# Kernel optimization log

Measured on AMD Instinct MI355X. Metric: run time of the kernel, lower is better.

The kernel has to match this reference:

```python
import jax, jax.numpy as jnp
import numpy as np

DIM = 1024
STATE = 256
B, S = 4, 4096

def setup_inputs() -> dict:
    key = jax.random.key(0)
    ks = jax.random.split(key, 8)
    sc_b = 1.0 / np.sqrt(DIM)
    sc_c = 1.0 / np.sqrt(STATE)
    return {
        "x": jax.random.normal(ks[0], (B, S, DIM), dtype=jnp.float32),
        "A": jax.random.normal(ks[1], (STATE,), dtype=jnp.float32) * 0.02,
        "B_w": jax.random.uniform(ks[2], (STATE, DIM), minval=-sc_b, maxval=sc_b),
        "B_b": jax.random.uniform(ks[3], (STATE,), minval=-sc_b, maxval=sc_b),
        "C_w": jax.random.uniform(ks[4], (DIM, STATE), minval=-sc_c, maxval=sc_c),
        "C_b": jax.random.uniform(ks[5], (DIM,), minval=-sc_c, maxval=sc_c),
        "D_w": jax.random.uniform(ks[6], (DIM, DIM), minval=-sc_b, maxval=sc_b),
        "D_b": jax.random.uniform(ks[7], (DIM,), minval=-sc_b, maxval=sc_b),
    }

def reference(x, A, B_w, B_b, C_w, C_b, D_w, D_b):
    # Precompute input projections in batch (the per-step loop only needs state*A + Bu)
    Bu = jnp.einsum('bsd,nd->bsn', x, B_w) + B_b          # [B,S,STATE]
    Du = jnp.einsum('bsd,ed->bse', x, D_w) + D_b          # [B,S,DIM]
    Aexp = jnp.exp(A)[None, :]                             # [1,STATE]
    state0 = jnp.zeros((x.shape[0], A.shape[0]), dtype=x.dtype)

    def step(state, bu_t):
        state = jnp.tanh(state * Aexp + bu_t)
        return state, state

    _, states = jax.lax.scan(step, state0, jnp.swapaxes(Bu, 0, 1))  # [S,B,STATE]
    states = jnp.swapaxes(states, 0, 1)                              # [B,S,STATE]
    y = jnp.einsum('bsn,en->bse', states, C_w) + C_b + Du
    return y
```

## Files before the change

### kernel.cpp

```cpp
#include <hip/hip_runtime.h>
#include <hip/hip_bf16.h>

#define DIM 1024
#define STATE 256
#define BATCH 4
#define SEQ 4096
#define M_TOT (BATCH * SEQ)

typedef short short8 __attribute__((ext_vector_type(8)));
typedef float f32x4 __attribute__((ext_vector_type(4)));

__device__ __forceinline__ unsigned short f2bf(float f) {
  unsigned int u = __float_as_uint(f);
  u += 0x7fff + ((u >> 16) & 1);
  return (unsigned short)(u >> 16);
}

__device__ __forceinline__ float bf2f(unsigned short u) {
  return __uint_as_float((unsigned int)u << 16);
}

__device__ __forceinline__ void gl_lds16(const void* g, void* l) {
  __builtin_amdgcn_global_load_lds(
      (const __attribute__((address_space(1))) void*)g,
      (__attribute__((address_space(3))) void*)l, 16, 0, 0);
}

#define C2F 2.8853900817779268f
#define LOG2EF 1.4426950408889634f
#define VMC(N) asm volatile("s_waitcnt vmcnt(" #N ")" ::: "memory")

__global__ __launch_bounds__(256) void convert_bw(
    const float* __restrict__ Bw, unsigned short* __restrict__ bwb) {
  const int r = blockIdx.x;
  const int c = threadIdx.x * 4;
  const float4 v = *(const float4*)(Bw + (size_t)r * DIM + c);
  *(ushort4*)(bwb + (size_t)r * DIM + c) =
      make_ushort4(f2bf(v.x), f2bf(v.y), f2bf(v.z), f2bf(v.w));
}

__global__ __launch_bounds__(256, 2) void gemm_GX(
    const float* __restrict__ x,
    const unsigned short* __restrict__ bwb,
    const float* __restrict__ Bb,
    const float* __restrict__ A,
    unsigned short* __restrict__ G,
    unsigned short* __restrict__ xb)
{
  __shared__ char lds[81920];

  const int tid = threadIdx.x;
  const int wave = tid >> 6;
  const int lane = tid & 63;
  const int lr = lane & 15;
  const int lk = lane >> 4;
  const int m0 = blockIdx.x * 32;

  f32x4 acc[2][4];
#pragma unroll
  for (int i = 0; i < 2; ++i)
#pragma unroll
    for (int j = 0; j < 4; ++j) acc[i][j] = (f32x4){0.f, 0.f, 0.f, 0.f};

  const char* xB  = (const char*)x;
  const char* bwB = (const char*)bwb;
  char* xbB = (char*)xb;

  auto stage = [&](int kt) {
    if (kt >= 16) return;
    char* slot = lds + (kt & 1) * 40960;
#pragma unroll
    for (int i = 0; i < 2; ++i) {
      const int s = i * 256 + tid;
      const int r = s >> 4;
      const int c = (s & 15) ^ (r & 7);
      gl_lds16(xB + (size_t)(m0 + r) * 4096 + (size_t)kt * 256 + c * 16,
               slot + i * 4096 + wave * 1024);
    }
#pragma unroll
    for (int i = 0; i < 8; ++i) {
      const int s = i * 256 + tid;
      const int r = s >> 3;
      const int c = (s & 7) ^ (r & 7);
      gl_lds16(bwB + (size_t)r * 2048 + (size_t)kt * 128 + c * 16,
               slot + 8192 + i * 4096 + wave * 1024);
    }
  };

  stage(0);
  VMC(0);
  __builtin_amdgcn_s_barrier();
  stage(1);

  for (int t = 0; t < 16; ++t) {
    const char* As = lds + (t & 1) * 40960;
    const char* Bs = As + 8192;

    short8 af[2][2];
#pragma unroll
    for (int kk = 0; kk < 2; ++kk)
#pragma unroll
      for (int f = 0; f < 2; ++f) {
        const int row = f * 16 + lr;
        const int sw = row & 7;
        const f32x4 a0 = *(const f32x4*)(As + row * 256 + (((kk * 8 + 2 * lk)     ^ sw) << 4));
        const f32x4 a1 = *(const f32x4*)(As + row * 256 + (((kk * 8 + 2 * lk + 1) ^ sw) << 4));
        short8 v;
#pragma unroll
        for (int j = 0; j < 4; ++j) {
          v[j]     = (short)f2bf(a0[j]);
          v[4 + j] = (short)f2bf(a1[j]);
        }
        af[kk][f] = v;
      }

    if ((t & 3) == wave) {
#pragma unroll
      for (int kk = 0; kk < 2; ++kk)
#pragma unroll
        for (int f = 0; f < 2; ++f) {
          const int row = f * 16 + lr;
          *(short8*)(xbB + (size_t)(m0 + row) * 2048 +
                     (size_t)t * 128 + kk * 64 + lk * 16) = af[kk][f];
        }
    }

    short8 bfr[2][4];
#pragma unroll
    for (int kk = 0; kk < 2; ++kk)
#pragma unroll
      for (int fj = 0; fj < 4; ++fj) {
        const int n = wave * 64 + fj * 16 + lr;
        bfr[kk][fj] = *(const short8*)(Bs + n * 128 + (((kk * 4 + lk) ^ (n & 7)) << 4));
      }
#pragma unroll
    for (int kk = 0; kk < 2; ++kk)
#pragma unroll
      for (int f = 0; f < 2; ++f)
#pragma unroll
        for (int fj = 0; fj < 4; ++fj)
          acc[f][fj] = __builtin_amdgcn_mfma_f32_16x16x32_bf16(
              af[kk][f], bfr[kk][fj], acc[f][fj], 0, 0, 0);

    if (t < 15) {
      VMC(0);
      __builtin_amdgcn_s_barrier();
      stage(t + 2);
    }
  }

#pragma unroll
  for (int fj = 0; fj < 4; ++fj) {
    const int cg = wave * 64 + fj * 16 + lr;
    const float bbv = fmaf(Bb[cg], C2F,
                           C2F * __builtin_amdgcn_exp2f(A[cg] * LOG2EF));
#pragma unroll
    for (int f = 0; f < 2; ++f)
#pragma unroll
      for (int j = 0; j < 4; ++j) {
        const int rg = m0 + f * 16 + lk * 4 + j;
        G[(size_t)rg * STATE + cg] = f2bf(fmaf(acc[f][fj][j], C2F, bbv));
      }
  }
}

__global__ __launch_bounds__(256) void scan_kernel(
    const unsigned short* __restrict__ G,
    const float* __restrict__ A,
    const float* __restrict__ Cw,
    const float* __restrict__ Dw,
    unsigned short* __restrict__ wob,
    unsigned short* __restrict__ states)
{
  const int tid = threadIdx.x;
  const int e0 = blockIdx.x * 4;
#pragma unroll
  for (int rr = 0; rr < 4; ++rr) {
    const int e = e0 + rr;
    if (tid < 64) {
      const float4 v = *(const float4*)(Cw + (size_t)e * STATE + tid * 4);
      *(ushort4*)(wob + (size_t)e * 1280 + tid * 4) =
          make_ushort4(f2bf(v.x), f2bf(v.y), f2bf(v.z), f2bf(v.w));
    }
    const float4 v = *(const float4*)(Dw + (size_t)e * DIM + tid * 4);
    *(ushort4*)(wob + (size_t)e * 1280 + 256 + tid * 4) =
        make_ushort4(f2bf(v.x), f2bf(v.y), f2bf(v.z), f2bf(v.w));
  }

  const int b = blockIdx.x >> 6;
  const int chunk = blockIdx.x & 63;
  const int n = tid;
  const int t0 = chunk * 64;
  const int start = (t0 > 64) ? (t0 - 64) : 0;
  const int nw = t0 - start;
  const int total = nw + 64;

  const unsigned short* g = G + ((size_t)b * SEQ + start) * STATE + n;
  unsigned short* q = states + ((size_t)b * SEQ + start) * STATE + n;
  const float P = C2F * __builtin_amdgcn_exp2f(A[n] * LOG2EF);
  const float mP2 = -2.0f * P;

  float r = 0.5f;
  constexpr int CH = 16;
  float cur[CH], nxt[CH];
#pragma unroll
  for (int j = 0; j < CH; ++j) cur[j] = bf2f(g[(size_t)j * STATE]);

  const int NC = total / CH;
  for (int c = 0; c < NC; ++c) {
    if (c + 1 < NC) {
      const unsigned short* pn = g + (size_t)(c + 1) * CH * STATE;
#pragma unroll
      for (int j = 0; j < CH; ++j) nxt[j] = bf2f(pn[(size_t)j * STATE]);
    }
    if (c * CH >= nw) {
      unsigned short* qc = q + (size_t)c * CH * STATE;
#pragma unroll
      for (int j = 0; j < CH; ++j) {
        const float t = fmaf(mP2, r, cur[j]);
        const float e = __builtin_amdgcn_exp2f(t);
        r = __builtin_amdgcn_rcpf(1.0f + e);
        const float s = fmaf(-2.0f, r, 1.0f);
        qc[(size_t)j * STATE] = f2bf(s);
      }
    } else {
#pragma unroll
      for (int j = 0; j < CH; ++j) {
        const float t = fmaf(mP2, r, cur[j]);
        const float e = __builtin_amdgcn_exp2f(t);
        r = __builtin_amdgcn_rcpf(1.0f + e);
      }
    }
    if (c + 1 < NC) {
#pragma unroll
      for (int j = 0; j < CH; ++j) cur[j] = nxt[j];
    }
  }
}

#define PH(TILE, Q, STG, VMST)                                                 \
  do {                                                                         \
    const char* As = lds + ((TILE) & 1) * 32768;                               \
    const char* Bs = lds + 65536 + ((TILE) & 1) * 32768;                       \
    if ((Q) == 0) {                                                            \
      _Pragma("unroll") for (int fj = 0; fj < 4; ++fj) {                       \
        const int r = wn * 64 + fj * 16 + lr;                                  \
        _Pragma("unroll") for (int kk = 0; kk < 2; ++kk)                       \
          bfr[fj][kk] = *(const short8*)(Bs + r * 128 +                        \
                                         (((kk * 4 + lk) ^ (r & 7)) << 4));    \
      }                                                                        \
    }                                                                          \
    short8 af[2][2];                                                           \
    _Pragma("unroll") for (int fl = 0; fl < 2; ++fl) {                         \
      const int r = wm * 128 + (Q) * 32 + fl * 16 + lr;                        \
      _Pragma("unroll") for (int kk = 0; kk < 2; ++kk)                         \
        af[fl][kk] = *(const short8*)(As + r * 128 +                           \
                                      (((kk * 4 + lk) ^ (r & 7)) << 4));       \
    }                                                                          \
    STG;                                                                       \
    if ((Q) == 0) asm volatile("s_waitcnt lgkmcnt(8)" ::: "memory");           \
    __builtin_amdgcn_s_barrier();                                              \
    __builtin_amdgcn_s_setprio(1);                                             \
    _Pragma("unroll") for (int kk = 0; kk < 2; ++kk)                           \
      _Pragma("unroll") for (int fl = 0; fl < 2; ++fl)                         \
        _Pragma("unroll") for (int fj = 0; fj < 4; ++fj)                       \
          acc[(Q) * 2 + fl][fj] = __builtin_amdgcn_mfma_f32_16x16x32_bf16(     \
              af[fl][kk], bfr[fj][kk], acc[(Q) * 2 + fl][fj], 0, 0, 0);        \
    __builtin_amdgcn_s_setprio(0);                                             \
    VMST;                                                                      \
    __builtin_amdgcn_s_barrier();                                              \
  } while (0)

__global__ __launch_bounds__(512, 2) void gemm_out(
    const unsigned short* __restrict__ stb,
    const unsigned short* __restrict__ xb,
    const unsigned short* __restrict__ wob,
    const float* __restrict__ Cb,
    const float* __restrict__ Db,
    float* __restrict__ dout)
{
  __shared__ char lds[131072];

  const int tid = threadIdx.x;
  const int wave = tid >> 6;
  const int lane = tid & 63;
  const int lr = lane & 15;
  const int lk = lane >> 4;
  const int wm = wave >> 2;
  const int wn = wave & 3;

  const int bs = ((blockIdx.x & 7) << 5) | (blockIdx.x >> 3);
  const int m0 = (bs >> 2) * 256;
  const int n0 = (bs & 3) * 256;

  const char* stbB = (const char*)stb;
  const char* xbB  = (const char*)xb;
  const char* wobB = (const char*)wob;

  f32x4 acc[8][4];
#pragma unroll
  for (int i = 0; i < 8; ++i)
#pragma unroll
    for (int j = 0; j < 4; ++j) acc[i][j] = (f32x4){0.f, 0.f, 0.f, 0.f};

  auto stageA = [&](int kt, int h) {
    if (kt >= 20) return;
    const char* base;
    size_t str;
    size_t colb;
    if (kt < 4) { base = stbB; str = 512;  colb = (size_t)kt * 128; }
    else        { base = xbB;  str = 2048; colb = (size_t)(kt - 4) * 128; }
    base += (size_t)m0 * str;
#pragma unroll
    for (int i2 = 0; i2 < 2; ++i2) {
      const int s = i2 * 512 + tid;
      const int r = s >> 3;
      const int cl = (s & 7) ^ (r & 7);
      gl_lds16(base + (size_t)(h * 128 + r) * str + colb + cl * 16,
               lds + ((kt & 1) * 32768) + h * 16384 + i2 * 8192 + wave * 1024);
    }
  };
  auto stageB = [&](int kt, int h) {
    if (kt >= 20) return;
#pragma unroll
    for (int i2 = 0; i2 < 2; ++i2) {
      const int s = i2 * 512 + tid;
      const int r = s >> 3;
      const int cl = (s & 7) ^ (r & 7);
      gl_lds16(wobB + (size_t)(n0 + h * 128 + r) * 2560 + (size_t)kt * 128 + cl * 16,
               lds + 65536 + ((kt & 1) * 32768) + h * 16384 + i2 * 8192 + wave * 1024);
    }
  };

  stageA(0, 0); stageA(0, 1);
  stageB(0, 0); stageB(0, 1);
  stageB(1, 0); stageB(1, 1);
  VMC(4);
  __builtin_amdgcn_s_barrier();

  short8 bfr[4][2];
  for (int i = 0; i < 10; ++i) {
    const int e = 2 * i, o = e + 1;
    PH(e, 0, stageA(o, 0), );
    PH(e, 1, stageA(o, 1), );
    PH(e, 2, stageB(e + 2, 0), );
    PH(e, 3, stageB(e + 2, 1), if (i == 9) { VMC(0); } else { VMC(4); });
    PH(o, 0, stageA(e + 2, 0), );
    PH(o, 1, stageA(e + 2, 1), );
    PH(o, 2, stageB(o + 2, 0), );
    PH(o, 3, stageB(o + 2, 1), VMC(4));
  }

#pragma unroll
  for (int fj = 0; fj < 4; ++fj) {
    const int col = n0 + wn * 64 + fj * 16 + lr;
    const float cb = Cb[col] + Db[col];
#pragma unroll
    for (int m = 0; m < 8; ++m) {
      const int rowb = m0 + wm * 128 + m * 16 + lk * 4;
#pragma unroll
      for (int j = 0; j < 4; ++j)
        dout[(size_t)(rowb + j) * DIM + col] = acc[m][fj][j] + cb;
    }
  }
}

extern "C" void kernel_launch(void* const* d_in, const int* in_sizes, int n_in,
                              void* d_out, int out_size, void* d_ws, size_t ws_size,
                              hipStream_t stream) {
  const float* x  = (const float*)d_in[0];
  const float* A  = (const float*)d_in[1];
  const float* Bw = (const float*)d_in[2];
  const float* Bb = (const float*)d_in[3];
  const float* Cw = (const float*)d_in[4];
  const float* Cb = (const float*)d_in[5];
  const float* Dw = (const float*)d_in[6];
  const float* Db = (const float*)d_in[7];
  float* dout = (float*)d_out;

  char* ws = (char*)d_ws;
  unsigned short* xb   = (unsigned short*)(ws);
  unsigned short* bwb  = (unsigned short*)(ws + 33554432);
  unsigned short* wob  = (unsigned short*)(ws + 34078720);
  unsigned short* G    = (unsigned short*)(ws + 36700160);
  unsigned short* stb  = (unsigned short*)(ws + 53477376);

  convert_bw<<<256, 256, 0, stream>>>(Bw, bwb);
  gemm_GX<<<512, 256, 0, stream>>>(x, bwb, Bb, A, G, xb);
  scan_kernel<<<BATCH * 64, 256, 0, stream>>>(G, A, Cw, Dw, wob, stb);
  gemm_out<<<256, 512, 0, stream>>>(stb, xb, wob, Cb, Db, dout);
}
```

Measured before the change: 91.04 us.

## Fuse chunked scan into output GEMM prologue and merge weight conversions

Removes the standalone scan kernel. Each output-GEMM block now recomputes the chunked tanh recurrence for its own 256 rows, with a 64-step warmup, writes the states to the workspace, then waits and barriers before its K loop reads them. The C/D weight conversion moves into the B-weight conversion kernel, so the pipeline has three launches instead of four. The cost is that the four column blocks sharing a row range each repeat the scan and write identical state values. Each block also runs a longer serial recurrence before any MFMA work, and correctness depends on the block's own global stores being visible to its later LDS-direct loads.

New measurement: 89.46 us. No clear change (-1.7%).

```diff
diff --git a/kernel.cpp b/kernel.cpp
--- a/kernel.cpp
+++ b/kernel.cpp
@@ -30,13 +30,32 @@
 #define LOG2EF 1.4426950408889634f
 #define VMC(N) asm volatile("s_waitcnt vmcnt(" #N ")" ::: "memory")
 
-__global__ __launch_bounds__(256) void convert_bw(
-    const float* __restrict__ Bw, unsigned short* __restrict__ bwb) {
-  const int r = blockIdx.x;
-  const int c = threadIdx.x * 4;
-  const float4 v = *(const float4*)(Bw + (size_t)r * DIM + c);
-  *(ushort4*)(bwb + (size_t)r * DIM + c) =
-      make_ushort4(f2bf(v.x), f2bf(v.y), f2bf(v.z), f2bf(v.w));
+__global__ __launch_bounds__(256) void convert_w(
+    const float* __restrict__ Bw, const float* __restrict__ Cw,
+    const float* __restrict__ Dw, unsigned short* __restrict__ bwb,
+    unsigned short* __restrict__ wob) {
+  const int bx = blockIdx.x;
+  const int t = threadIdx.x;
+  if (bx < 256) {
+    const int c = t * 4;
+    const float4 v = *(const float4*)(Bw + (size_t)bx * DIM + c);
+    *(ushort4*)(bwb + (size_t)bx * DIM + c) =
+        make_ushort4(f2bf(v.x), f2bf(v.y), f2bf(v.z), f2bf(v.w));
+  } else {
+    const int e0 = (bx - 256) * 4;
+#pragma unroll
+    for (int rr = 0; rr < 4; ++rr) {
+      const int e = e0 + rr;
+      if (t < 64) {
+        const float4 v = *(const float4*)(Cw + (size_t)e * STATE + t * 4);
+        *(ushort4*)(wob + (size_t)e * 1280 + t * 4) =
+            make_ushort4(f2bf(v.x), f2bf(v.y), f2bf(v.z), f2bf(v.w));
+      }
+      const float4 v = *(const float4*)(Dw + (size_t)e * DIM + t * 4);
+      *(ushort4*)(wob + (size_t)e * 1280 + 256 + t * 4) =
+          make_ushort4(f2bf(v.x), f2bf(v.y), f2bf(v.z), f2bf(v.w));
+    }
+  }
 }
 
 __global__ __launch_bounds__(256, 2) void gemm_GX(
@@ -161,80 +180,6 @@
         const int rg = m0 + f * 16 + lk * 4 + j;
         G[(size_t)rg * STATE + cg] = f2bf(fmaf(acc[f][fj][j], C2F, bbv));
       }
-  }
-}
-
-__global__ __launch_bounds__(256) void scan_kernel(
-    const unsigned short* __restrict__ G,
-    const float* __restrict__ A,
-    const float* __restrict__ Cw,
-    const float* __restrict__ Dw,
-    unsigned short* __restrict__ wob,
-    unsigned short* __restrict__ states)
-{
-  const int tid = threadIdx.x;
-  const int e0 = blockIdx.x * 4;
-#pragma unroll
-  for (int rr = 0; rr < 4; ++rr) {
-    const int e = e0 + rr;
-    if (tid < 64) {
-      const float4 v = *(const float4*)(Cw + (size_t)e * STATE + tid * 4);
-      *(ushort4*)(wob + (size_t)e * 1280 + tid * 4) =
-          make_ushort4(f2bf(v.x), f2bf(v.y), f2bf(v.z), f2bf(v.w));
-    }
-    const float4 v = *(const float4*)(Dw + (size_t)e * DIM + tid * 4);
-    *(ushort4*)(wob + (size_t)e * 1280 + 256 + tid * 4) =
-        make_ushort4(f2bf(v.x), f2bf(v.y), f2bf(v.z), f2bf(v.w));
-  }
-
-  const int b = blockIdx.x >> 6;
-  const int chunk = blockIdx.x & 63;
-  const int n = tid;
-  const int t0 = chunk * 64;
-  const int start = (t0 > 64) ? (t0 - 64) : 0;
-  const int nw = t0 - start;
-  const int total = nw + 64;
-
-  const unsigned short* g = G + ((size_t)b * SEQ + start) * STATE + n;
-  unsigned short* q = states + ((size_t)b * SEQ + start) * STATE + n;
-  const float P = C2F * __builtin_amdgcn_exp2f(A[n] * LOG2EF);
-  const float mP2 = -2.0f * P;
-
-  float r = 0.5f;
-  constexpr int CH = 16;
-  float cur[CH], nxt[CH];
-#pragma unroll
-  for (int j = 0; j < CH; ++j) cur[j] = bf2f(g[(size_t)j * STATE]);
-
-  const int NC = total / CH;
-  for (int c = 0; c < NC; ++c) {
-    if (c + 1 < NC) {
-      const unsigned short* pn = g + (size_t)(c + 1) * CH * STATE;
-#pragma unroll
-      for (int j = 0; j < CH; ++j) nxt[j] = bf2f(pn[(size_t)j * STATE]);
-    }
-    if (c * CH >= nw) {
-      unsigned short* qc = q + (size_t)c * CH * STATE;
-#pragma unroll
-      for (int j = 0; j < CH; ++j) {
-        const float t = fmaf(mP2, r, cur[j]);
-        const float e = __builtin_amdgcn_exp2f(t);
-        r = __builtin_amdgcn_rcpf(1.0f + e);
-        const float s = fmaf(-2.0f, r, 1.0f);
-        qc[(size_t)j * STATE] = f2bf(s);
-      }
-    } else {
-#pragma unroll
-      for (int j = 0; j < CH; ++j) {
-        const float t = fmaf(mP2, r, cur[j]);
-        const float e = __builtin_amdgcn_exp2f(t);
-        r = __builtin_amdgcn_rcpf(1.0f + e);
-      }
-    }
-    if (c + 1 < NC) {
-#pragma unroll
-      for (int j = 0; j < CH; ++j) cur[j] = nxt[j];
-    }
   }
 }
 
@@ -272,9 +217,11 @@
   } while (0)
 
 __global__ __launch_bounds__(512, 2) void gemm_out(
-    const unsigned short* __restrict__ stb,
+    const unsigned short* __restrict__ G,
+    unsigned short* __restrict__ stb,
     const unsigned short* __restrict__ xb,
     const unsigned short* __restrict__ wob,
+    const float* __restrict__ Aarr,
     const float* __restrict__ Cb,
     const float* __restrict__ Db,
     float* __restrict__ dout)
@@ -292,6 +239,59 @@
   const int bs = ((blockIdx.x & 7) << 5) | (blockIdx.x >> 3);
   const int m0 = (bs >> 2) * 256;
   const int n0 = (bs & 3) * 256;
+
+  {
+    const int c2 = tid >> 8;
+    const int n  = tid & 255;
+    const int T0 = m0 & 4095;
+    const int startT = (c2 == 0) ? ((T0 == 0) ? 0 : T0 - 64) : T0 + 64;
+    const int nw = (c2 == 0 && T0 == 0) ? 0 : 64;
+    const int total = nw + 128;
+    const int mstart = (m0 - T0) + startT;
+    const unsigned short* g = G + (size_t)mstart * STATE + n;
+    unsigned short* q = stb + (size_t)mstart * STATE + n;
+    const float P = C2F * __builtin_amdgcn_exp2f(Aarr[n] * LOG2EF);
+    const float mP2 = -2.0f * P;
+
+    float r = 0.5f;
+    constexpr int CH = 16;
+    float cur[CH], nxt[CH];
+#pragma unroll
+    for (int j = 0; j < CH; ++j) cur[j] = bf2f(g[(size_t)j * STATE]);
+
+    const int NC = total / CH;
+    for (int c = 0; c < NC; ++c) {
+      if (c + 1 < NC) {
+        const unsigned short* pn = g + (size_t)(c + 1) * CH * STATE;
+#pragma unroll
+        for (int j = 0; j < CH; ++j) nxt[j] = bf2f(pn[(size_t)j * STATE]);
+      }
+      if (c * CH >= nw) {
+        unsigned short* qc = q + (size_t)c * CH * STATE;
+#pragma unroll
+        for (int j = 0; j < CH; ++j) {
+          const float t = fmaf(mP2, r, cur[j]);
+          const float e = __builtin_amdgcn_exp2f(t);
+          r = __builtin_amdgcn_rcpf(1.0f + e);
+          const float s = fmaf(-2.0f, r, 1.0f);
+          qc[(size_t)j * STATE] = f2bf(s);
+        }
+      } else {
+#pragma unroll
+        for (int j = 0; j < CH; ++j) {
+          const float t = fmaf(mP2, r, cur[j]);
+          const float e = __builtin_amdgcn_exp2f(t);
+          r = __builtin_amdgcn_rcpf(1.0f + e);
+        }
+      }
+      if (c + 1 < NC) {
+#pragma unroll
+        for (int j = 0; j < CH; ++j) cur[j] = nxt[j];
+      }
+    }
+  }
+  VMC(0);
+  __builtin_amdgcn_s_barrier();
 
   const char* stbB = (const char*)stb;
   const char* xbB  = (const char*)xb;
@@ -385,8 +385,7 @@
   unsigned short* G    = (unsigned short*)(ws + 36700160);
   unsigned short* stb  = (unsigned short*)(ws + 53477376);
 
-  convert_bw<<<256, 256, 0, stream>>>(Bw, bwb);
+  convert_w<<<512, 256, 0, stream>>>(Bw, Cw, Dw, bwb, wob);
   gemm_GX<<<512, 256, 0, stream>>>(x, bwb, Bb, A, G, xb);
-  scan_kernel<<<BATCH * 64, 256, 0, stream>>>(G, A, Cw, Dw, wob, stb);
-  gemm_out<<<256, 512, 0, stream>>>(stb, xb, wob, Cb, Db, dout);
-}
+  gemm_out<<<256, 512, 0, stream>>>(G, stb, xb, wob, A, Cb, Db, dout);
+}
```
